# Optimization experiments

Hardware: AMD Instinct MI355X
Metric: run time of the kernel (lower is better)

## Reference

```python
import jax, jax.numpy as jnp
import numpy as np

N, V, T, C_IN, C_OUT, REL, H4, H5 = 256, 25, 128, 64, 64, 9, 18, 6


def setup_inputs() -> dict:
    key = jax.random.key(0)
    ks = jax.random.split(key, 12)

    def w(k, shape, fan_in):
        return (jax.random.normal(k, shape, jnp.float32) / np.sqrt(fan_in)).astype(jnp.float32)

    return {
        "x": jax.random.normal(ks[0], (N, V, T, C_IN), jnp.float32),
        "A": jax.random.uniform(ks[1], (V, V), dtype=jnp.float32),
        "W1": w(ks[2], (C_IN, REL), C_IN), "b1": jnp.zeros((REL,), jnp.float32),
        "W2": w(ks[3], (C_IN, REL), C_IN), "b2": jnp.zeros((REL,), jnp.float32),
        "W3": w(ks[4], (C_IN, REL), C_IN), "b3": jnp.zeros((REL,), jnp.float32),
        "W4a": w(ks[5], (REL, H4), REL), "b4a": jnp.zeros((H4,), jnp.float32),
        "W4b": w(ks[6], (H4, REL), H4), "b4b": jnp.zeros((REL,), jnp.float32),
        "W5a": w(ks[7], (REL, H5), REL), "b5a": jnp.zeros((H5,), jnp.float32),
        "W5b": w(ks[8], (H5, C_OUT), H5), "b5b": jnp.zeros((C_OUT,), jnp.float32),
    }


def reference(x, A, W1, b1, W2, b2, W3, b3, W4a, b4a, W4b, b4b, W5a, b5a, W5b, b5b):
    silu = jax.nn.silu
    alpha = 1.0
    # x: (N, V, T, C) channels-last; Linear projections to rel channels
    x1 = x @ W1 + b1                       # (N, V, T, R)
    x2 = x @ W2 + b2                       # (N, V, T, R)
    x3 = x @ W3 + b3                       # (N, V, T, R)
    # temporal mean (original: transpose(1,3).mean(-2))
    m1 = x1.mean(axis=2)                   # (N, V, R)
    m2 = x2.mean(axis=2)                   # (N, V, R)
    # pairwise joint affinity via broadcast difference
    rel = m1[:, :, None, :] - m2[:, None, :, :]   # (N, V, V, R)
    # small MLP (Linear4) on channel dim
    h = silu(rel @ W4a + b4a)              # (N, V, V, 18)
    h = silu(h @ W4b + b4b)                # (N, V, V, R)
    # scale + static adjacency (broadcast over batch and channels)
    h = h * alpha + A[None, :, :, None]    # (N, V, V, R)
    # einsum 'ncuv,nctv->nctu' in channels-last form: aggregate over v
    agg = jnp.einsum('nuvc,nvtc->nutc', h, x3)    # (N, V, T, R)
    # output MLP (Linear5)
    y = silu(agg @ W5a + b5a)              # (N, V, T, 6)
    y = silu(y @ W5b + b5b)                # (N, V, T, C_out)
    return y
```

## Files before the change

### kernel.cpp

```cpp
#include <hip/hip_runtime.h>
#include <hip/hip_fp16.h>

#define NN 256
#define VV 25
#define TT 128
#define CIN 64
#define CO 64
#define RR 9
#define HH4 18
#define HH5 6
#define TQ 32
#define NT (TT / TQ)

typedef unsigned int uint32;

__device__ __forceinline__ float silu_f(float v) {
  return __fdividef(v, 1.0f + __expf(-v));
}

__global__ __launch_bounds__(128) void k1_proj(
    const float* __restrict__ x, const float* __restrict__ W3,
    const float* __restrict__ b3, __half* __restrict__ x3h,
    float* __restrict__ xm) {
  const int blk = blockIdx.x;
  const int tid = threadIdx.x;
  __shared__ float xt[TT][65];
  __shared__ float xmp[2][64];

  const float* xs = x + (size_t)blk * TT * CIN;
  float4 r[16];
  #pragma unroll
  for (int k = 0; k < 16; ++k) r[k] = ((const float4*)xs)[k * 128 + tid];
  #pragma unroll
  for (int k = 0; k < 16; ++k) {
    const int idx = k * 128 + tid;
    const int t = idx >> 4;
    const int c = (idx & 15) * 4;
    xt[t][c + 0] = r[k].x; xt[t][c + 1] = r[k].y;
    xt[t][c + 2] = r[k].z; xt[t][c + 3] = r[k].w;
  }
  __syncthreads();

  float acc[RR];
  #pragma unroll
  for (int c = 0; c < RR; ++c) acc[c] = b3[c];
  #pragma unroll 8
  for (int c = 0; c < CIN; ++c) {
    const float xv = xt[tid][c];
    #pragma unroll
    for (int j = 0; j < RR; ++j) acc[j] = fmaf(xv, W3[c * RR + j], acc[j]);
  }
  {
    union { __half h[12]; uint2 u2[3]; } row;
    #pragma unroll
    for (int j = 0; j < RR; ++j) row.h[j] = __float2half(acc[j]);
    row.h[9] = __float2half(0.f); row.h[10] = __float2half(0.f);
    row.h[11] = __float2half(0.f);
    uint2* dst = (uint2*)(x3h + ((size_t)blk * TT + tid) * 12);
    dst[0] = row.u2[0]; dst[1] = row.u2[1]; dst[2] = row.u2[2];
  }

  {
    const int c = tid & 63, hh = tid >> 6;
    float s = 0.f;
    #pragma unroll
    for (int j = 0; j < 64; ++j) s += xt[hh * 64 + j][c];
    xmp[hh][c] = s;
  }
  __syncthreads();
  if (tid < 64) xm[(size_t)blk * 64 + tid] = xmp[0][tid] + xmp[1][tid];
}

__global__ __launch_bounds__(128) void k2_h(
    const float* __restrict__ xm, const float* __restrict__ A,
    const float* __restrict__ W1, const float* __restrict__ b1,
    const float* __restrict__ W2, const float* __restrict__ b2,
    const float* __restrict__ W4a, const float* __restrict__ b4a,
    const float* __restrict__ W4b, const float* __restrict__ b4b,
    __half2* __restrict__ h2) {
  const int n = blockIdx.x;
  const int tid = threadIdx.x;
  __shared__ float m1[VV][RR];
  __shared__ float m2[VV][RR];
  const float* xmn = xm + (size_t)n * VV * CIN;
  for (int i = tid; i < 2 * VV * RR; i += 128) {
    const int which = (i >= VV * RR);
    const int idx = which ? i - VV * RR : i;
    const int v = idx / RR, c = idx % RR;
    const float* W = which ? W2 : W1;
    const float* b = which ? b2 : b1;
    const float* row = xmn + v * CIN;
    float s = 0.f;
    #pragma unroll
    for (int k = 0; k < CIN; ++k) s = fmaf(row[k], W[k * RR + c], s);
    s = s * (1.0f / TT) + b[c];
    if (which) m2[v][c] = s; else m1[v][c] = s;
  }
  __syncthreads();
  for (int p = tid; p < VV * VV; p += 128) {
    const int u = p / VV, v2 = p % VV;
    float r[RR];
    #pragma unroll
    for (int c = 0; c < RR; ++c) r[c] = m1[u][c] - m2[v2][c];
    float t1[HH4];
    #pragma unroll
    for (int j = 0; j < HH4; ++j) {
      float s = b4a[j];
      #pragma unroll
      for (int c = 0; c < RR; ++c) s = fmaf(r[c], W4a[c * HH4 + j], s);
      t1[j] = silu_f(s);
    }
    const float av = A[u * VV + v2];
    float hc[RR];
    #pragma unroll
    for (int c = 0; c < RR; ++c) {
      float s = b4b[c];
      #pragma unroll
      for (int j = 0; j < HH4; ++j) s = fmaf(t1[j], W4b[j * RR + c], s);
      hc[c] = silu_f(s) + av;
    }
    __half2* hp = h2 + ((size_t)n * VV * VV + p) * 5;
    hp[0] = __floats2half2_rn(hc[0], hc[1]);
    hp[1] = __floats2half2_rn(hc[2], hc[3]);
    hp[2] = __floats2half2_rn(hc[4], hc[5]);
    hp[3] = __floats2half2_rn(hc[6], hc[7]);
    hp[4] = __floats2half2_rn(hc[8], 0.f);
  }
}

__global__ __launch_bounds__(256) void k3_out(
    const __half* __restrict__ x3h, const __half2* __restrict__ h2,
    const float* __restrict__ W5a, const float* __restrict__ b5a,
    const float* __restrict__ W5b, const float* __restrict__ b5b,
    float* __restrict__ out) {
  const int bid = blockIdx.x;
  const int n = bid >> 2, tq = bid & (NT - 1);
  const int tid = threadIdx.x;
  __shared__ __half2 x3s[VV * TQ * 6];
  __shared__ __half2 h2s[VV * VV * 5];
  __shared__ __half2 a5s[VV * TQ * 3];

  for (int i = tid; i < VV * 192; i += 256) {
    const int v = i / 192, rr = i - v * 192;
    const uint32* src =
        (const uint32*)(x3h + (((size_t)(n * VV + v)) * TT + tq * TQ) * 12);
    ((uint32*)x3s)[v * 192 + rr] = src[rr];
  }
  {
    const uint32* src = (const uint32*)(h2 + (size_t)n * VV * VV * 5);
    for (int i = tid; i < VV * VV * 5; i += 256) ((uint32*)h2s)[i] = src[i];
  }
  __syncthreads();

  for (int p = tid; p < VV * TQ; p += 256) {
    const int u = p >> 5, t = p & (TQ - 1);
    __half2 a0 = __floats2half2_rn(0.f, 0.f), a1 = a0, a2 = a0, a3 = a0, a4 = a0;
    const __half2* hr = h2s + u * VV * 5;
    const __half2* xr = x3s + t * 6;
    #pragma unroll 5
    for (int v = 0; v < VV; ++v) {
      const __half2* hv = hr + v * 5;
      const __half2* xv = xr + v * TQ * 6;
      a0 = __hfma2(hv[0], xv[0], a0);
      a1 = __hfma2(hv[1], xv[1], a1);
      a2 = __hfma2(hv[2], xv[2], a2);
      a3 = __hfma2(hv[3], xv[3], a3);
      a4 = __hfma2(hv[4], xv[4], a4);
    }
    float ag[RR];
    ag[0] = __low2float(a0); ag[1] = __high2float(a0);
    ag[2] = __low2float(a1); ag[3] = __high2float(a1);
    ag[4] = __low2float(a2); ag[5] = __high2float(a2);
    ag[6] = __low2float(a3); ag[7] = __high2float(a3);
    ag[8] = __low2float(a4);
    float a5v[HH5];
    #pragma unroll
    for (int j = 0; j < HH5; ++j) {
      float s = b5a[j];
      #pragma unroll
      for (int c = 0; c < RR; ++c) s = fmaf(ag[c], W5a[c * HH5 + j], s);
      a5v[j] = silu_f(s);
    }
    a5s[p * 3 + 0] = __floats2half2_rn(a5v[0], a5v[1]);
    a5s[p * 3 + 1] = __floats2half2_rn(a5v[2], a5v[3]);
    a5s[p * 3 + 2] = __floats2half2_rn(a5v[4], a5v[5]);
  }
  __syncthreads();

  const int cq = (tid & 15) * 4;
  float4 wb[HH5];
  #pragma unroll
  for (int j = 0; j < HH5; ++j) wb[j] = *(const float4*)(W5b + j * CO + cq);
  const float4 bb = *(const float4*)(b5b + cq);
  #pragma unroll 2
  for (int it = 0; it < (VV * TQ) / 16; ++it) {
    const int q = it * 16 + (tid >> 4);
    const int u = q >> 5, t = q & (TQ - 1);
    const __half2 p01 = a5s[q * 3 + 0];
    const __half2 p23 = a5s[q * 3 + 1];
    const __half2 p45 = a5s[q * 3 + 2];
    const float a0 = __low2float(p01), a1 = __high2float(p01);
    const float a2 = __low2float(p23), a3 = __high2float(p23);
    const float a4 = __low2float(p45), a5 = __high2float(p45);
    float4 y;
    y.x = silu_f(bb.x + a0 * wb[0].x + a1 * wb[1].x + a2 * wb[2].x +
                 a3 * wb[3].x + a4 * wb[4].x + a5 * wb[5].x);
    y.y = silu_f(bb.y + a0 * wb[0].y + a1 * wb[1].y + a2 * wb[2].y +
                 a3 * wb[3].y + a4 * wb[4].y + a5 * wb[5].y);
    y.z = silu_f(bb.z + a0 * wb[0].z + a1 * wb[1].z + a2 * wb[2].z +
                 a3 * wb[3].z + a4 * wb[4].z + a5 * wb[5].z);
    y.w = silu_f(bb.w + a0 * wb[0].w + a1 * wb[1].w + a2 * wb[2].w +
                 a3 * wb[3].w + a4 * wb[4].w + a5 * wb[5].w);
    float* orow = out + ((size_t)(n * VV + u) * TT + tq * TQ + t) * CO + cq;
    *(float4*)orow = y;
  }
}

extern "C" void kernel_launch(void* const* d_in, const int* in_sizes, int n_in,
                              void* d_out, int out_size, void* d_ws, size_t ws_size,
                              hipStream_t stream) {
  const float* x   = (const float*)d_in[0];
  const float* A   = (const float*)d_in[1];
  const float* W1  = (const float*)d_in[2];
  const float* b1  = (const float*)d_in[3];
  const float* W2  = (const float*)d_in[4];
  const float* b2  = (const float*)d_in[5];
  const float* W3  = (const float*)d_in[6];
  const float* b3  = (const float*)d_in[7];
  const float* W4a = (const float*)d_in[8];
  const float* b4a = (const float*)d_in[9];
  const float* W4b = (const float*)d_in[10];
  const float* b4b = (const float*)d_in[11];
  const float* W5a = (const float*)d_in[12];
  const float* b5a = (const float*)d_in[13];
  const float* W5b = (const float*)d_in[14];
  const float* b5b = (const float*)d_in[15];

  char* ws = (char*)d_ws;
  __half* x3h  = (__half*)ws;
  float*  xm   = (float*)(ws + 19660800);
  __half2* h2  = (__half2*)(ws + 19660800 + 1638400);
  float* out = (float*)d_out;

  hipLaunchKernelGGL(k1_proj, dim3(NN * VV), dim3(128), 0, stream, x, W3, b3, x3h, xm);
  hipLaunchKernelGGL(k2_h, dim3(NN), dim3(128), 0, stream,
                     xm, A, W1, b1, W2, b2, W4a, b4a, W4b, b4b, h2);
  hipLaunchKernelGGL(k3_out, dim3(NN * NT), dim3(256), 0, stream,
                     x3h, h2, W5a, b5a, W5b, b5b, out);
}
```

Baseline: 164.1 us.

## Reorder x3 intermediate into per-block tiles and vectorize shared-memory access

k1 now writes the fp16 x3 projection in a layout grouped by (n, time-quarter, v, t), so each k3 block can copy its tile with contiguous uint4 loads instead of strided per-row gathers. k1 computes the temporal channel sum from registers with wavefront shuffles instead of a second shared-memory pass, and uses float4 shared-memory rows. h is padded to 6 words so k3's inner loop can use uint2 shared-memory loads, and launch-bounds occupancy hints are added. The padding slightly increases h traffic and shared-memory use, and the occupancy hints may constrain register allocation.

```diff
diff --git a/kernel.cpp b/kernel.cpp
--- a/kernel.cpp
+++ b/kernel.cpp
@@ -10,65 +10,79 @@
 #define HH4 18
 #define HH5 6
 #define TQ 32
-#define NT (TT / TQ)
-
-typedef unsigned int uint32;
+#define NT 4
+
+typedef unsigned int uint;
 
 __device__ __forceinline__ float silu_f(float v) {
   return __fdividef(v, 1.0f + __expf(-v));
 }
-
-__global__ __launch_bounds__(128) void k1_proj(
+__device__ __forceinline__ __half2 u2h(uint u) {
+  union { uint x; __half2 h; } c; c.x = u; return c.h;
+}
+__device__ __forceinline__ uint h2u(__half2 h) {
+  union { __half2 h; uint x; } c; c.h = h; return c.x;
+}
+
+__global__ __launch_bounds__(128, 2) void k1_proj(
     const float* __restrict__ x, const float* __restrict__ W3,
-    const float* __restrict__ b3, __half* __restrict__ x3h,
+    const float* __restrict__ b3, uint* __restrict__ x3g,
     float* __restrict__ xm) {
   const int blk = blockIdx.x;
+  const int n = blk / VV, v = blk - n * VV;
   const int tid = threadIdx.x;
-  __shared__ float xt[TT][65];
-  __shared__ float xmp[2][64];
-
-  const float* xs = x + (size_t)blk * TT * CIN;
+  __shared__ __align__(16) float xt[TT * 68];
+  __shared__ __align__(16) float xmp[2][64];
+
+  const float4* src = (const float4*)(x + (size_t)blk * TT * CIN);
   float4 r[16];
   #pragma unroll
-  for (int k = 0; k < 16; ++k) r[k] = ((const float4*)xs)[k * 128 + tid];
+  for (int k = 0; k < 16; ++k) r[k] = src[k * 128 + tid];
   #pragma unroll
   for (int k = 0; k < 16; ++k) {
     const int idx = k * 128 + tid;
-    const int t = idx >> 4;
-    const int c = (idx & 15) * 4;
-    xt[t][c + 0] = r[k].x; xt[t][c + 1] = r[k].y;
-    xt[t][c + 2] = r[k].z; xt[t][c + 3] = r[k].w;
-  }
-  __syncthreads();
+    const int t = idx >> 4, c = (idx & 15) * 4;
+    *(float4*)(xt + t * 68 + c) = r[k];
+  }
+  float4 cs = r[0];
+  #pragma unroll
+  for (int k = 1; k < 16; ++k) {
+    cs.x += r[k].x; cs.y += r[k].y; cs.z += r[k].z; cs.w += r[k].w;
+  }
+  #pragma unroll
+  for (int m = 16; m < 64; m <<= 1) {
+    cs.x += __shfl_xor(cs.x, m); cs.y += __shfl_xor(cs.y, m);
+    cs.z += __shfl_xor(cs.z, m); cs.w += __shfl_xor(cs.w, m);
+  }
+  if ((tid & 63) < 16) *(float4*)(&xmp[tid >> 6][(tid & 15) * 4]) = cs;
+  __syncthreads();
+  if (tid < 64) xm[(size_t)blk * 64 + tid] = xmp[0][tid] + xmp[1][tid];
 
   float acc[RR];
   #pragma unroll
-  for (int c = 0; c < RR; ++c) acc[c] = b3[c];
-  #pragma unroll 8
-  for (int c = 0; c < CIN; ++c) {
-    const float xv = xt[tid][c];
-    #pragma unroll
-    for (int j = 0; j < RR; ++j) acc[j] = fmaf(xv, W3[c * RR + j], acc[j]);
-  }
-  {
-    union { __half h[12]; uint2 u2[3]; } row;
-    #pragma unroll
-    for (int j = 0; j < RR; ++j) row.h[j] = __float2half(acc[j]);
-    row.h[9] = __float2half(0.f); row.h[10] = __float2half(0.f);
-    row.h[11] = __float2half(0.f);
-    uint2* dst = (uint2*)(x3h + ((size_t)blk * TT + tid) * 12);
-    dst[0] = row.u2[0]; dst[1] = row.u2[1]; dst[2] = row.u2[2];
-  }
-
-  {
-    const int c = tid & 63, hh = tid >> 6;
-    float s = 0.f;
-    #pragma unroll
-    for (int j = 0; j < 64; ++j) s += xt[hh * 64 + j][c];
-    xmp[hh][c] = s;
-  }
-  __syncthreads();
-  if (tid < 64) xm[(size_t)blk * 64 + tid] = xmp[0][tid] + xmp[1][tid];
+  for (int j = 0; j < RR; ++j) acc[j] = b3[j];
+  const float* xrow = xt + tid * 68;
+  #pragma unroll
+  for (int c4 = 0; c4 < 16; ++c4) {
+    const float4 xv = *(const float4*)(xrow + c4 * 4);
+    #pragma unroll
+    for (int j = 0; j < RR; ++j) {
+      acc[j] = fmaf(xv.x, W3[(c4 * 4 + 0) * RR + j], acc[j]);
+      acc[j] = fmaf(xv.y, W3[(c4 * 4 + 1) * RR + j], acc[j]);
+      acc[j] = fmaf(xv.z, W3[(c4 * 4 + 2) * RR + j], acc[j]);
+      acc[j] = fmaf(xv.w, W3[(c4 * 4 + 3) * RR + j], acc[j]);
+    }
+  }
+  uint w0 = h2u(__floats2half2_rn(acc[0], acc[1]));
+  uint w1 = h2u(__floats2half2_rn(acc[2], acc[3]));
+  uint w2 = h2u(__floats2half2_rn(acc[4], acc[5]));
+  uint w3 = h2u(__floats2half2_rn(acc[6], acc[7]));
+  uint w4 = h2u(__floats2half2_rn(acc[8], 0.f));
+  uint* dst = x3g +
+      ((((size_t)n * NT + (tid >> 5)) * VV + v) * TQ + (tid & 31)) * 6;
+  ((uint2*)dst)[0] = make_uint2(w0, w1);
+  ((uint2*)dst)[1] = make_uint2(w2, w3);
+  ((uint2*)dst)[2] = make_uint2(w4, 0u);
 }
 
 __global__ __launch_bounds__(128) void k2_h(
@@ -77,16 +91,16 @@
     const float* __restrict__ W2, const float* __restrict__ b2,
     const float* __restrict__ W4a, const float* __restrict__ b4a,
     const float* __restrict__ W4b, const float* __restrict__ b4b,
-    __half2* __restrict__ h2) {
+    uint* __restrict__ h2g) {
   const int n = blockIdx.x;
   const int tid = threadIdx.x;
-  __shared__ float m1[VV][RR];
-  __shared__ float m2[VV][RR];
+  __shared__ float m1[VV][RR + 1];
+  __shared__ float m2[VV][RR + 1];
   const float* xmn = xm + (size_t)n * VV * CIN;
   for (int i = tid; i < 2 * VV * RR; i += 128) {
     const int which = (i >= VV * RR);
     const int idx = which ? i - VV * RR : i;
-    const int v = idx / RR, c = idx % RR;
+    const int v = idx / RR, c = idx - v * RR;
     const float* W = which ? W2 : W1;
     const float* b = which ? b2 : b1;
     const float* row = xmn + v * CIN;
@@ -98,107 +112,106 @@
   }
   __syncthreads();
   for (int p = tid; p < VV * VV; p += 128) {
-    const int u = p / VV, v2 = p % VV;
-    float r[RR];
-    #pragma unroll
-    for (int c = 0; c < RR; ++c) r[c] = m1[u][c] - m2[v2][c];
+    const int u = p / VV, v2 = p - u * VV;
+    float rel[RR];
+    #pragma unroll
+    for (int j = 0; j < RR; ++j) rel[j] = m1[u][j] - m2[v2][j];
     float t1[HH4];
     #pragma unroll
-    for (int j = 0; j < HH4; ++j) {
-      float s = b4a[j];
+    for (int k = 0; k < HH4; ++k) {
+      float s = b4a[k];
       #pragma unroll
-      for (int c = 0; c < RR; ++c) s = fmaf(r[c], W4a[c * HH4 + j], s);
-      t1[j] = silu_f(s);
+      for (int j = 0; j < RR; ++j) s = fmaf(rel[j], W4a[j * HH4 + k], s);
+      t1[k] = silu_f(s);
     }
     const float av = A[u * VV + v2];
     float hc[RR];
     #pragma unroll
-    for (int c = 0; c < RR; ++c) {
-      float s = b4b[c];
+    for (int j = 0; j < RR; ++j) {
+      float s = b4b[j];
       #pragma unroll
-      for (int j = 0; j < HH4; ++j) s = fmaf(t1[j], W4b[j * RR + c], s);
-      hc[c] = silu_f(s) + av;
-    }
-    __half2* hp = h2 + ((size_t)n * VV * VV + p) * 5;
-    hp[0] = __floats2half2_rn(hc[0], hc[1]);
-    hp[1] = __floats2half2_rn(hc[2], hc[3]);
-    hp[2] = __floats2half2_rn(hc[4], hc[5]);
-    hp[3] = __floats2half2_rn(hc[6], hc[7]);
-    hp[4] = __floats2half2_rn(hc[8], 0.f);
-  }
-}
-
-__global__ __launch_bounds__(256) void k3_out(
-    const __half* __restrict__ x3h, const __half2* __restrict__ h2,
+      for (int k = 0; k < HH4; ++k) s = fmaf(t1[k], W4b[k * RR + j], s);
+      hc[j] = silu_f(s) + av;
+    }
+    uint* hp = h2g + ((size_t)n * VV * VV + p) * 6;
+    hp[0] = h2u(__floats2half2_rn(hc[0], hc[1]));
+    hp[1] = h2u(__floats2half2_rn(hc[2], hc[3]));
+    hp[2] = h2u(__floats2half2_rn(hc[4], hc[5]));
+    hp[3] = h2u(__floats2half2_rn(hc[6], hc[7]));
+    hp[4] = h2u(__floats2half2_rn(hc[8], 0.f));
+    hp[5] = 0u;
+  }
+}
+
+__global__ __launch_bounds__(256, 3) void k3_out(
+    const uint* __restrict__ x3g, const uint* __restrict__ h2g,
     const float* __restrict__ W5a, const float* __restrict__ b5a,
     const float* __restrict__ W5b, const float* __restrict__ b5b,
     float* __restrict__ out) {
   const int bid = blockIdx.x;
-  const int n = bid >> 2, tq = bid & (NT - 1);
+  const int n = bid >> 2, tq = bid & 3;
   const int tid = threadIdx.x;
-  __shared__ __half2 x3s[VV * TQ * 6];
-  __shared__ __half2 h2s[VV * VV * 5];
-  __shared__ __half2 a5s[VV * TQ * 3];
-
-  for (int i = tid; i < VV * 192; i += 256) {
-    const int v = i / 192, rr = i - v * 192;
-    const uint32* src =
-        (const uint32*)(x3h + (((size_t)(n * VV + v)) * TT + tq * TQ) * 12);
-    ((uint32*)x3s)[v * 192 + rr] = src[rr];
-  }
-  {
-    const uint32* src = (const uint32*)(h2 + (size_t)n * VV * VV * 5);
-    for (int i = tid; i < VV * VV * 5; i += 256) ((uint32*)h2s)[i] = src[i];
-  }
+  __shared__ __align__(16) uint x3s[VV * TQ * 6];
+  __shared__ __align__(16) uint h2s[VV * VV * 6];
+  __shared__ __align__(16) uint a5s[VV * TQ * 3];
+
+  const uint* xsrc = x3g + (size_t)bid * (VV * TQ * 6);
+  for (int i = tid; i < (VV * TQ * 6) / 4; i += 256)
+    ((uint4*)x3s)[i] = ((const uint4*)xsrc)[i];
+  const uint* hsrc = h2g + (size_t)n * (VV * VV * 6);
+  for (int i = tid; i < VV * VV * 6; i += 256) h2s[i] = hsrc[i];
   __syncthreads();
 
   for (int p = tid; p < VV * TQ; p += 256) {
-    const int u = p >> 5, t = p & (TQ - 1);
-    __half2 a0 = __floats2half2_rn(0.f, 0.f), a1 = a0, a2 = a0, a3 = a0, a4 = a0;
-    const __half2* hr = h2s + u * VV * 5;
-    const __half2* xr = x3s + t * 6;
+    const int u = p >> 5, t = p & 31;
+    const uint* xr = x3s + t * 6;
+    const uint* hr = h2s + u * VV * 6;
+    __half2 c0 = u2h(0u), c1 = c0, c2 = c0, c3 = c0, c4 = c0;
     #pragma unroll 5
-    for (int v = 0; v < VV; ++v) {
-      const __half2* hv = hr + v * 5;
-      const __half2* xv = xr + v * TQ * 6;
-      a0 = __hfma2(hv[0], xv[0], a0);
-      a1 = __hfma2(hv[1], xv[1], a1);
-      a2 = __hfma2(hv[2], xv[2], a2);
-      a3 = __hfma2(hv[3], xv[3], a3);
-      a4 = __hfma2(hv[4], xv[4], a4);
+    for (int v2 = 0; v2 < VV; ++v2) {
+      const uint2 xa = *(const uint2*)(xr + v2 * 192);
+      const uint2 xb = *(const uint2*)(xr + v2 * 192 + 2);
+      const uint  xc = xr[v2 * 192 + 4];
+      const uint2 ha = *(const uint2*)(hr + v2 * 6);
+      const uint2 hb = *(const uint2*)(hr + v2 * 6 + 2);
+      const uint  hc = hr[v2 * 6 + 4];
+      c0 = __hfma2(u2h(ha.x), u2h(xa.x), c0);
+      c1 = __hfma2(u2h(ha.y), u2h(xa.y), c1);
+      c2 = __hfma2(u2h(hb.x), u2h(xb.x), c2);
+      c3 = __hfma2(u2h(hb.y), u2h(xb.y), c3);
+      c4 = __hfma2(u2h(hc),   u2h(xc),   c4);
     }
     float ag[RR];
-    ag[0] = __low2float(a0); ag[1] = __high2float(a0);
-    ag[2] = __low2float(a1); ag[3] = __high2float(a1);
-    ag[4] = __low2float(a2); ag[5] = __high2float(a2);
-    ag[6] = __low2float(a3); ag[7] = __high2float(a3);
-    ag[8] = __low2float(a4);
+    ag[0] = __low2float(c0); ag[1] = __high2float(c0);
+    ag[2] = __low2float(c1); ag[3] = __high2float(c1);
+    ag[4] = __low2float(c2); ag[5] = __high2float(c2);
+    ag[6] = __low2float(c3); ag[7] = __high2float(c3);
+    ag[8] = __low2float(c4);
     float a5v[HH5];
     #pragma unroll
-    for (int j = 0; j < HH5; ++j) {
-      float s = b5a[j];
+    for (int k = 0; k < HH5; ++k) {
+      float s = b5a[k];
       #pragma unroll
-      for (int c = 0; c < RR; ++c) s = fmaf(ag[c], W5a[c * HH5 + j], s);
-      a5v[j] = silu_f(s);
-    }
-    a5s[p * 3 + 0] = __floats2half2_rn(a5v[0], a5v[1]);
-    a5s[p * 3 + 1] = __floats2half2_rn(a5v[2], a5v[3]);
-    a5s[p * 3 + 2] = __floats2half2_rn(a5v[4], a5v[5]);
+      for (int j = 0; j < RR; ++j) s = fmaf(ag[j], W5a[j * HH5 + k], s);
+      a5v[k] = silu_f(s);
+    }
+    a5s[p * 3 + 0] = h2u(__floats2half2_rn(a5v[0], a5v[1]));
+    a5s[p * 3 + 1] = h2u(__floats2half2_rn(a5v[2], a5v[3]));
+    a5s[p * 3 + 2] = h2u(__floats2half2_rn(a5v[4], a5v[5]));
   }
   __syncthreads();
 
   const int cq = (tid & 15) * 4;
   float4 wb[HH5];
   #pragma unroll
-  for (int j = 0; j < HH5; ++j) wb[j] = *(const float4*)(W5b + j * CO + cq);
+  for (int k = 0; k < HH5; ++k) wb[k] = *(const float4*)(W5b + k * CO + cq);
   const float4 bb = *(const float4*)(b5b + cq);
-  #pragma unroll 2
   for (int it = 0; it < (VV * TQ) / 16; ++it) {
     const int q = it * 16 + (tid >> 4);
-    const int u = q >> 5, t = q & (TQ - 1);
-    const __half2 p01 = a5s[q * 3 + 0];
-    const __half2 p23 = a5s[q * 3 + 1];
-    const __half2 p45 = a5s[q * 3 + 2];
+    const int u = q >> 5, t = q & 31;
+    const __half2 p01 = u2h(a5s[q * 3 + 0]);
+    const __half2 p23 = u2h(a5s[q * 3 + 1]);
+    const __half2 p45 = u2h(a5s[q * 3 + 2]);
     const float a0 = __low2float(p01), a1 = __high2float(p01);
     const float a2 = __low2float(p23), a3 = __high2float(p23);
     const float a4 = __low2float(p45), a5 = __high2float(p45);
@@ -211,7 +224,8 @@
                  a3 * wb[3].z + a4 * wb[4].z + a5 * wb[5].z);
     y.w = silu_f(bb.w + a0 * wb[0].w + a1 * wb[1].w + a2 * wb[2].w +
                  a3 * wb[3].w + a4 * wb[4].w + a5 * wb[5].w);
-    float* orow = out + ((size_t)(n * VV + u) * TT + tq * TQ + t) * CO + cq;
+    float* orow = out +
+        ((size_t)(n * VV + u) * TT + tq * TQ + t) * CO + cq;
     *(float4*)orow = y;
   }
 }
@@ -235,16 +249,17 @@
   const float* b5a = (const float*)d_in[13];
   const float* W5b = (const float*)d_in[14];
   const float* b5b = (const float*)d_in[15];
+  float* out = (float*)d_out;
 
   char* ws = (char*)d_ws;
-  __half* x3h  = (__half*)ws;
-  float*  xm   = (float*)(ws + 19660800);
-  __half2* h2  = (__half2*)(ws + 19660800 + 1638400);
-  float* out = (float*)d_out;
-
-  hipLaunchKernelGGL(k1_proj, dim3(NN * VV), dim3(128), 0, stream, x, W3, b3, x3h, xm);
+  uint*  x3g = (uint*)ws;
+  float* xm  = (float*)(ws + 19660800);
+  uint*  h2g = (uint*)(ws + 19660800 + 1638400);
+
+  hipLaunchKernelGGL(k1_proj, dim3(NN * VV), dim3(128), 0, stream,
+                     x, W3, b3, x3g, xm);
   hipLaunchKernelGGL(k2_h, dim3(NN), dim3(128), 0, stream,
-                     xm, A, W1, b1, W2, b2, W4a, b4a, W4b, b4b, h2);
+                     xm, A, W1, b1, W2, b2, W4a, b4a, W4b, b4b, h2g);
   hipLaunchKernelGGL(k3_out, dim3(NN * NT), dim3(256), 0, stream,
-                     x3h, h2, W5a, b5a, W5b, b5b, out);
-}
+                     x3g, h2g, W5a, b5a, W5b, b5b, out);
+}
```

Result: no change. 162.2 us (-1.2%).
